# Performance work log

Hardware: AMD Instinct MI355X
Metric: run time of the kernel (lower is better)

Reference implementation:

```python
import jax, jax.numpy as jnp
import numpy as np

NUM_GRAPHS = 64


def gcn_conv(x, src, dst, num_nodes, W, b):
    # PyG GCNConv: linear first, then normalized aggregation, bias after.
    h = x @ W  # [N, out]
    # degree with self-loops already included in (src, dst)
    deg = jax.ops.segment_sum(jnp.ones_like(src, dtype=h.dtype), dst, num_segments=num_nodes)
    dinv = jnp.where(deg > 0, jax.lax.rsqrt(jnp.maximum(deg, 1e-12)), 0.0)
    norm = dinv[src] * dinv[dst]  # [E]
    msg = h[src] * norm[:, None]  # [E, out] gather + scale
    out = jax.ops.segment_sum(msg, dst, num_segments=num_nodes)  # scatter-add
    return out + b


def setup_inputs() -> dict:
    key = jax.random.key(0)
    ks = jax.random.split(key, 12)
    N, E = 50000, 400000
    dims = [36, 75, 150, 50]
    x = jax.random.normal(ks[0], (N, dims[0]), dtype=jnp.float32)
    edge_index = jax.random.randint(ks[1], (2, E), 0, N, dtype=jnp.int64)
    batch = jnp.sort(jax.random.randint(ks[2], (N,), 0, NUM_GRAPHS, dtype=jnp.int64))
    def glorot(k, fi, fo):
        lim = np.sqrt(6.0 / (fi + fo)).astype(np.float32)
        return jax.random.uniform(k, (fi, fo), jnp.float32, -lim, lim)
    inp = {"x": x, "edge_index": edge_index, "batch": batch}
    for i in range(3):
        inp[f"W{i+1}"] = glorot(ks[3 + 2 * i], dims[i], dims[i + 1])
        inp[f"b{i+1}"] = jnp.zeros((dims[i + 1],), jnp.float32)
    inp["Wo"] = glorot(ks[9], dims[3], 3)
    inp["bo"] = jnp.zeros((3,), jnp.float32)
    return inp


def reference(x, edge_index, batch, W1, b1, W2, b2, W3, b3, Wo, bo):
    N = x.shape[0]
    loop = jnp.arange(N, dtype=edge_index.dtype)
    src = jnp.concatenate([edge_index[0], loop])  # add self-loops
    dst = jnp.concatenate([edge_index[1], loop])
    h = x
    for W, b in ((W1, b1), (W2, b2), (W3, b3)):
        h = gcn_conv(h, src, dst, N, W, b)
        h = jax.nn.relu(h)  # dropout is identity in eval mode
    h = h @ Wo + bo  # [N, 3]
    pooled = jax.ops.segment_max(h, batch, num_segments=NUM_GRAPHS)  # [G, 3]
    return jax.nn.softmax(pooled, axis=1)
```

## Files before the change

### kernel.cpp

```cpp
#include <hip/hip_runtime.h>
#include <hip/hip_bf16.h>

#define DIV_UP(a, b) (((a) + (b) - 1) / (b))
typedef long long ll;
typedef __attribute__((ext_vector_type(8))) short short8;
typedef __attribute__((ext_vector_type(4))) float f32x4;

__device__ __forceinline__ float ldf(const void* p, ll i, int bf) {
    return bf ? __bfloat162float(((const __hip_bfloat16*)p)[i]) : ((const float*)p)[i];
}
__device__ __forceinline__ int ldi(const int* p, ll i, int w) {
    return w ? p[2 * i] : p[i];
}
template <int MODE>
__device__ __forceinline__ float ldm(const void* p, ll i, int bf) {
    if (MODE == 1) return __bfloat162float(((const __hip_bfloat16*)p)[i]);
    return ldf(p, i, bf);
}
__device__ __forceinline__ void bf16pair(unsigned u, float& f0, float& f1) {
    f0 = __uint_as_float(u << 16);
    f1 = __uint_as_float(u & 0xFFFF0000u);
}

__device__ __forceinline__ unsigned fenc(float f) {
    unsigned u = __float_as_uint(f);
    return (u & 0x80000000u) ? ~u : (u | 0x80000000u);
}
__device__ __forceinline__ float fdec(unsigned u) {
    unsigned v = (u & 0x80000000u) ? (u & 0x7FFFFFFFu) : ~u;
    return __uint_as_float(v);
}
#define ENC_NEG_INF 0x007FFFFFu

#define MB1 0
#define MB2 80
#define MHW 240
#define MB3 390
#define MBO 440
#define N_MISC 444
#define P1 0
#define P2 5120
#define P3 20480
#define N_PACK 30720

__global__ void k_detect(const unsigned* __restrict__ xb, const unsigned* __restrict__ eb,
                         int* __restrict__ flags, int* __restrict__ cnt, int N) {
    int idx = blockIdx.x * 256 + threadIdx.x;
    if (idx < N) cnt[idx] = 0;
    if (blockIdx.x != 0) return;
    __shared__ int sv[2];
    int t = threadIdx.x;
    if (t < 2) sv[t] = 0;
    __syncthreads();
    unsigned e = (xb[t] >> 7) & 0xFFu;
    int vote = (e >= 115u && e <= 133u) ? 1 : 0;
    int zero = (eb[2 * t + 1] == 0u) ? 1 : 0;
    atomicAdd(&sv[0], vote);
    atomicAdd(&sv[1], zero);
    __syncthreads();
    if (t == 0) {
        flags[0] = (sv[0] > 128) ? 1 : 0;
        flags[1] = (sv[1] > 200) ? 1 : 0;
    }
}

__global__ void k_cvt(const void* __restrict__ W1, const void* __restrict__ b1,
                      const void* __restrict__ W2, const void* __restrict__ b2,
                      const void* __restrict__ W3, const void* __restrict__ b3,
                      const void* __restrict__ Wo, const void* __restrict__ bo,
                      __hip_bfloat16* __restrict__ wp, float* __restrict__ wfm,
                      const int* __restrict__ flags) {
    int t = blockIdx.x * blockDim.x + threadIdx.x;
    int bf = flags[0];
    if (t < N_PACK) {
        const void* W;
        int i, K, OUT, KC;
        if (t < P2) {
            W = W1;
            i = t;
            K = 36;
            OUT = 75;
            KC = 2;
        } else if (t < P3) {
            W = W2;
            i = t - P2;
            K = 75;
            OUT = 150;
            KC = 3;
        } else {
            W = W3;
            i = t - P3;
            K = 150;
            OUT = 50;
            KC = 5;
        }
        int j = i & 7;
        int lane = (i >> 3) & 63;
        int tile = i >> 9;
        int kc = tile % KC;
        int ct = tile / KC;
        int k = kc * 32 + ((lane >> 4) << 3) + j;
        int col = ct * 16 + (lane & 15);
        float v = (k < K && col < OUT) ? ldf(W, (ll)k * OUT + col, bf) : 0.0f;
        wp[t] = __float2bfloat16(v);
    } else {
        int m = t - N_PACK;
        if (m >= N_MISC) return;
        float v = 0.0f;
        if (m < 75)
            v = ldf(b1, m, bf);
        else if (m >= MB2 && m < MB2 + 150)
            v = ldf(b2, m - MB2, bf);
        else if (m >= MHW && m < MHW + 150)
            v = ldf(Wo, m - MHW, bf);
        else if (m >= MB3 && m < MB3 + 50)
            v = ldf(b3, m - MB3, bf);
        else if (m >= MBO && m < MBO + 3)
            v = ldf(bo, m - MBO, bf);
        wfm[m] = v;
    }
}

__global__ void k_hist(const int* __restrict__ ei, int* __restrict__ cnt,
                       const int* __restrict__ flags, int E) {
    int t = blockIdx.x * blockDim.x + threadIdx.x;
    if (t >= E) return;
    atomicAdd(&cnt[ldi(ei, (ll)E + t, flags[1])], 1);
}
__global__ void k_scan1(const int* __restrict__ cnt, int* __restrict__ bsum,
                        float* __restrict__ dinv, int N) {
    __shared__ int s[256];
    int t = threadIdx.x;
    int idx = blockIdx.x * 256 + t;
    int v = (idx < N) ? cnt[idx] : 0;
    if (idx < N) dinv[idx] = rsqrtf((float)v + 1.0f);
    s[t] = v;
    __syncthreads();
#pragma unroll
    for (int off = 128; off > 0; off >>= 1) {
        if (t < off) s[t] += s[t + off];
        __syncthreads();
    }
    if (t == 0) bsum[blockIdx.x] = s[0];
}
__global__ void k_scan2(int* __restrict__ bsum, int nb, unsigned* __restrict__ pooled) {
    __shared__ int s[256];
    int t = threadIdx.x;
    if (t < 192) pooled[t] = ENC_NEG_INF;
    int run = 0;
    for (int base = 0; base < nb; base += 256) {
        int i = base + t;
        int v = (i < nb) ? bsum[i] : 0;
        s[t] = v;
        __syncthreads();
        for (int off = 1; off < 256; off <<= 1) {
            int o = (t >= off) ? s[t - off] : 0;
            __syncthreads();
            s[t] += o;
            __syncthreads();
        }
        if (i < nb) bsum[i] = run + s[t] - v;
        run += s[255];
        __syncthreads();
    }
}
__global__ void k_scan3(int* __restrict__ cnt, const int* __restrict__ bsum,
                        int* __restrict__ rowptr, int N) {
    __shared__ int s[256];
    int t = threadIdx.x;
    int idx = blockIdx.x * 256 + t;
    int v = (idx < N) ? cnt[idx] : 0;
    if (idx < N) cnt[idx] = 0;
    s[t] = v;
    __syncthreads();
    for (int off = 1; off < 256; off <<= 1) {
        int o = (t >= off) ? s[t - off] : 0;
        __syncthreads();
        s[t] += o;
        __syncthreads();
    }
    if (idx <= N) rowptr[idx] = bsum[blockIdx.x] + s[t] - v;
}
__global__ void k_fill(const int* __restrict__ ei, const int* __restrict__ rowptr,
                       int* __restrict__ cursor, int2* __restrict__ ep,
                       const float* __restrict__ dinv, const int* __restrict__ flags, int E) {
    int t = blockIdx.x * blockDim.x + threadIdx.x;
    if (t >= E) return;
    int wi = flags[1];
    int s = ldi(ei, t, wi);
    int d = ldi(ei, (ll)E + t, wi);
    int pos = rowptr[d] + atomicAdd(&cursor[d], 1);
    int2 v;
    v.x = s;
    v.y = __float_as_int(dinv[s] * dinv[d]);
    ep[pos] = v;
}

__global__ void k_agg(const void* __restrict__ X, int xstride, __hip_bfloat16* __restrict__ Y,
                      int ystride, int C, const int* __restrict__ rowptr,
                      const int2* __restrict__ ep, const float* __restrict__ dinv,
                      const int* __restrict__ flags, int N) {
    int n = blockIdx.x * 4 + (threadIdx.x >> 6);
    if (n >= N) return;
    int lane = threadIdx.x & 63;
    int bf = flags[0];
    float di = dinv[n];
    float w0 = di * di;
    if (lane >= C) return;
    float a0 = w0 * ldm<2>(X, (ll)n * xstride + lane, bf);
    int j = rowptr[n];
    int je = rowptr[n + 1];
    for (; j + 3 < je; j += 4) {
        int2 v0 = ep[j];
        int2 v1 = ep[j + 1];
        int2 v2 = ep[j + 2];
        int2 v3 = ep[j + 3];
        a0 = fmaf(__int_as_float(v0.y), ldm<2>(X, (ll)v0.x * xstride + lane, bf), a0);
        a0 = fmaf(__int_as_float(v1.y), ldm<2>(X, (ll)v1.x * xstride + lane, bf), a0);
        a0 = fmaf(__int_as_float(v2.y), ldm<2>(X, (ll)v2.x * xstride + lane, bf), a0);
        a0 = fmaf(__int_as_float(v3.y), ldm<2>(X, (ll)v3.x * xstride + lane, bf), a0);
    }
    for (; j < je; ++j) {
        int2 v0 = ep[j];
        a0 = fmaf(__int_as_float(v0.y), ldm<2>(X, (ll)v0.x * xstride + lane, bf), a0);
    }
    Y[(ll)n * ystride + lane] = __float2bfloat16(a0);
}

__global__ void k_aggp(const __hip_bfloat16* __restrict__ X, int xs,
                       __hip_bfloat16* __restrict__ Y, int ys, int CP,
                       const int* __restrict__ rowptr, const int2* __restrict__ ep,
                       const float* __restrict__ dinv, int N) {
    int n = blockIdx.x * 4 + (threadIdx.x >> 6);
    if (n >= N) return;
    int lane = threadIdx.x & 63;
    if (lane >= CP) return;
    float di = dinv[n];
    float w0 = di * di;
    float a0, a1;
    {
        unsigned u = *(const unsigned*)(X + (ll)n * xs + 2 * lane);
        float f0, f1;
        bf16pair(u, f0, f1);
        a0 = w0 * f0;
        a1 = w0 * f1;
    }
    int j = rowptr[n];
    int je = rowptr[n + 1];
    for (; j + 3 < je; j += 4) {
        int2 v0 = ep[j];
        int2 v1 = ep[j + 1];
        int2 v2 = ep[j + 2];
        int2 v3 = ep[j + 3];
        unsigned u0 = *(const unsigned*)(X + (ll)v0.x * xs + 2 * lane);
        unsigned u1 = *(const unsigned*)(X + (ll)v1.x * xs + 2 * lane);
        unsigned u2 = *(const unsigned*)(X + (ll)v2.x * xs + 2 * lane);
        unsigned u3 = *(const unsigned*)(X + (ll)v3.x * xs + 2 * lane);
        float f0, f1;
        bf16pair(u0, f0, f1);
        float wa = __int_as_float(v0.y);
        a0 = fmaf(wa, f0, a0);
        a1 = fmaf(wa, f1, a1);
        bf16pair(u1, f0, f1);
        wa = __int_as_float(v1.y);
        a0 = fmaf(wa, f0, a0);
        a1 = fmaf(wa, f1, a1);
        bf16pair(u2, f0, f1);
        wa = __int_as_float(v2.y);
        a0 = fmaf(wa, f0, a0);
        a1 = fmaf(wa, f1, a1);
        bf16pair(u3, f0, f1);
        wa = __int_as_float(v3.y);
        a0 = fmaf(wa, f0, a0);
        a1 = fmaf(wa, f1, a1);
    }
    for (; j < je; ++j) {
        int2 v0 = ep[j];
        unsigned u = *(const unsigned*)(X + (ll)v0.x * xs + 2 * lane);
        float f0, f1;
        bf16pair(u, f0, f1);
        float wa = __int_as_float(v0.y);
        a0 = fmaf(wa, f0, a0);
        a1 = fmaf(wa, f1, a1);
    }
    __hip_bfloat162 h;
    h.x = __float2bfloat16(a0);
    h.y = __float2bfloat16(a1);
    *(__hip_bfloat162*)(Y + (ll)n * ys + 2 * lane) = h;
}

__global__ void k_agg3h(const __hip_bfloat16* __restrict__ X, int xs, float* __restrict__ zb,
                        const int* __restrict__ rowptr, const int2* __restrict__ ep,
                        const float* __restrict__ dinv, const float* __restrict__ wfm, int N) {
    int n = blockIdx.x * 4 + (threadIdx.x >> 6);
    if (n >= N) return;
    int lane = threadIdx.x & 63;
    bool act = lane < 25;
    int c0 = 2 * lane;
    float w00 = 0, w01 = 0, w02 = 0, w10 = 0, w11 = 0, w12 = 0, bb0 = 0, bb1 = 0;
    if (act) {
        w00 = wfm[MHW + c0 * 3 + 0];
        w01 = wfm[MHW + c0 * 3 + 1];
        w02 = wfm[MHW + c0 * 3 + 2];
        w10 = wfm[MHW + c0 * 3 + 3];
        w11 = wfm[MHW + c0 * 3 + 4];
        w12 = wfm[MHW + c0 * 3 + 5];
        bb0 = wfm[MB3 + c0];
        bb1 = wfm[MB3 + c0 + 1];
    }
    float di = dinv[n];
    float w0 = di * di;
    float a0 = 0.0f, a1 = 0.0f;
    if (act) {
        unsigned u = *(const unsigned*)(X + (ll)n * xs + 2 * lane);
        float f0, f1;
        bf16pair(u, f0, f1);
        a0 = w0 * f0;
        a1 = w0 * f1;
    }
    int j = rowptr[n];
    int je = rowptr[n + 1];
    for (; j + 3 < je; j += 4) {
        int2 v0 = ep[j];
        int2 v1 = ep[j + 1];
        int2 v2 = ep[j + 2];
        int2 v3 = ep[j + 3];
        if (act) {
            unsigned u0 = *(const unsigned*)(X + (ll)v0.x * xs + 2 * lane);
            unsigned u1 = *(const unsigned*)(X + (ll)v1.x * xs + 2 * lane);
            unsigned u2 = *(const unsigned*)(X + (ll)v2.x * xs + 2 * lane);
            unsigned u3 = *(const unsigned*)(X + (ll)v3.x * xs + 2 * lane);
            float f0, f1;
            bf16pair(u0, f0, f1);
            float wa = __int_as_float(v0.y);
            a0 = fmaf(wa, f0, a0);
            a1 = fmaf(wa, f1, a1);
            bf16pair(u1, f0, f1);
            wa = __int_as_float(v1.y);
            a0 = fmaf(wa, f0, a0);
            a1 = fmaf(wa, f1, a1);
            bf16pair(u2, f0, f1);
            wa = __int_as_float(v2.y);
            a0 = fmaf(wa, f0, a0);
            a1 = fmaf(wa, f1, a1);
            bf16pair(u3, f0, f1);
            wa = __int_as_float(v3.y);
            a0 = fmaf(wa, f0, a0);
            a1 = fmaf(wa, f1, a1);
        }
    }
    for (; j < je; ++j) {
        int2 v0 = ep[j];
        if (act) {
            unsigned u = *(const unsigned*)(X + (ll)v0.x * xs + 2 * lane);
            float f0, f1;
            bf16pair(u, f0, f1);
            float wa = __int_as_float(v0.y);
            a0 = fmaf(wa, f0, a0);
            a1 = fmaf(wa, f1, a1);
        }
    }
    float h0 = act ? fmaxf(a0 + bb0, 0.0f) : 0.0f;
    float h1 = act ? fmaxf(a1 + bb1, 0.0f) : 0.0f;
    float z0 = h0 * w00 + h1 * w10;
    float z1 = h0 * w01 + h1 * w11;
    float z2 = h0 * w02 + h1 * w12;
#pragma unroll
    for (int off = 32; off > 0; off >>= 1) {
        z0 += __shfl_xor(z0, off);
        z1 += __shfl_xor(z1, off);
        z2 += __shfl_xor(z2, off);
    }
    if (lane == 0) {
        zb[(ll)n * 3 + 0] = z0 + wfm[MBO + 0];
        zb[(ll)n * 3 + 1] = z1 + wfm[MBO + 1];
        zb[(ll)n * 3 + 2] = z2 + wfm[MBO + 2];
    }
}

template <int K, int KC, int OUT, int CT, bool RELU, bool BIAS>
__global__ __launch_bounds__(256) void k_gemm(const __hip_bfloat16* __restrict__ X, int xs,
                                              __hip_bfloat16* __restrict__ Y, int ys,
                                              const short8* __restrict__ Wp,
                                              const float* __restrict__ bias, int N) {
    const int lane = threadIdx.x & 63;
    const int wid = threadIdx.x >> 6;
    const int m0 = blockIdx.x * 64 + wid * 16;
    const int mrow = lane & 15;
    const int koct = lane >> 4;
    const __hip_bfloat16* xrow = X + (ll)(m0 + mrow) * xs + koct * 8;
    f32x4 acc[CT];
#pragma unroll
    for (int ct = 0; ct < CT; ++ct)
#pragma unroll
        for (int r = 0; r < 4; ++r) acc[ct][r] = 0.0f;
    float bv[CT];
#pragma unroll
    for (int ct = 0; ct < CT; ++ct) {
        int col = ct * 16 + mrow;
        bv[ct] = (BIAS && col < OUT) ? bias[col] : 0.0f;
    }
#pragma unroll 1
    for (int kc = 0; kc < KC; ++kc) {
        short8 a = *(const short8*)(xrow + kc * 32);
#pragma unroll
        for (int ct = 0; ct < CT; ++ct) {
            short8 b = Wp[(ct * KC + kc) * 64 + lane];
            acc[ct] = __builtin_amdgcn_mfma_f32_16x16x32_bf16(a, b, acc[ct], 0, 0, 0);
        }
    }
#pragma unroll
    for (int ct = 0; ct < CT; ++ct) {
        int col = ct * 16 + mrow;
        if (col >= OUT) continue;
#pragma unroll
        for (int r = 0; r < 4; ++r) {
            int node = m0 + koct * 4 + r;
            if (node >= N) continue;
            float v = acc[ct][r] + bv[ct];
            if (RELU) v = fmaxf(v, 0.0f);
            Y[(ll)node * ys + col] = __float2bfloat16(v);
        }
    }
}

__global__ void k_pool(const float* __restrict__ zb, const int* __restrict__ batch,
                       unsigned* __restrict__ pooled, const int* __restrict__ flags, int N) {
    __shared__ unsigned lmax[192];
    int wi = flags[1];
    for (int i = threadIdx.x; i < 192; i += blockDim.x) lmax[i] = ENC_NEG_INF;
    __syncthreads();
    int n = blockIdx.x * blockDim.x + threadIdx.x;
    int lane = threadIdx.x & 63;
    float z0 = -3.4e38f, z1 = -3.4e38f, z2 = -3.4e38f;
    int g = 0;
    if (n < N) {
        z0 = zb[(ll)n * 3 + 0];
        z1 = zb[(ll)n * 3 + 1];
        z2 = zb[(ll)n * 3 + 2];
        g = ldi(batch, n, wi);
    }
    int g0 = __shfl(g, 0);
    unsigned long long uni = __ballot(n < N && g == g0);
    if (uni == ~0ULL) {
#pragma unroll
        for (int off = 32; off > 0; off >>= 1) {
            z0 = fmaxf(z0, __shfl_xor(z0, off));
            z1 = fmaxf(z1, __shfl_xor(z1, off));
            z2 = fmaxf(z2, __shfl_xor(z2, off));
        }
        if (lane == 0) {
            atomicMax(&lmax[g0 * 3 + 0], fenc(z0));
            atomicMax(&lmax[g0 * 3 + 1], fenc(z1));
            atomicMax(&lmax[g0 * 3 + 2], fenc(z2));
        }
    } else if (n < N) {
        atomicMax(&lmax[g * 3 + 0], fenc(z0));
        atomicMax(&lmax[g * 3 + 1], fenc(z1));
        atomicMax(&lmax[g * 3 + 2], fenc(z2));
    }
    __syncthreads();
    for (int i = threadIdx.x; i < 192; i += blockDim.x) {
        unsigned v = lmax[i];
        if (v != ENC_NEG_INF) atomicMax(&pooled[i], v);
    }
}

__global__ void k_softmax(const unsigned* __restrict__ pooled, void* __restrict__ out,
                          const int* __restrict__ flags) {
    int g = threadIdx.x;
    if (g >= 64) return;
    int bf = flags[0];
    float a = fdec(pooled[g * 3 + 0]);
    float b = fdec(pooled[g * 3 + 1]);
    float c = fdec(pooled[g * 3 + 2]);
    float m = fmaxf(a, fmaxf(b, c));
    float ea = __expf(a - m), eb = __expf(b - m), ec = __expf(c - m);
    float s = 1.0f / (ea + eb + ec);
    if (bf) {
        __hip_bfloat16* o = (__hip_bfloat16*)out;
        o[g * 3 + 0] = __float2bfloat16(ea * s);
        o[g * 3 + 1] = __float2bfloat16(eb * s);
        o[g * 3 + 2] = __float2bfloat16(ec * s);
    } else {
        float* o = (float*)out;
        o[g * 3 + 0] = ea * s;
        o[g * 3 + 1] = eb * s;
        o[g * 3 + 2] = ec * s;
    }
}

extern "C" void kernel_launch(void* const* d_in, const int* in_sizes, int n_in,
                              void* d_out, int out_size, void* d_ws, size_t ws_size,
                              hipStream_t stream) {
    const void* x = d_in[0];
    const int* ei = (const int*)d_in[1];
    const int* batch = (const int*)d_in[2];

    const int N = in_sizes[0] / 36;
    const int E = in_sizes[1] / 2;

    char* ws = (char*)d_ws;
    size_t off = 0;
    auto carve = [&](size_t bytes) {
        char* p = ws + off;
        off = (off + bytes + 255) & ~(size_t)255;
        return p;
    };
    int* flags = (int*)carve(16);
    float* wfm = (float*)carve((size_t)N_MISC * 4);
    __hip_bfloat16* wpack = (__hip_bfloat16*)carve((size_t)N_PACK * 2);
    float* dinv = (float*)carve((size_t)N * 4);
    int* cnt = (int*)carve((size_t)N * 4);
    int* rowptr = (int*)carve((size_t)(N + 1) * 4);
    int2* ep = (int2*)carve((size_t)E * 8);
    unsigned* pooled = (unsigned*)carve(768);
    const int NB = DIV_UP(N + 1, 256);
    int* bsum = (int*)carve((size_t)NB * 4);
    float* zbuf = (float*)carve((size_t)N * 12);
    char* R1 = carve((size_t)N * 192);
    char* R2 = carve((size_t)N * 320);
    (void)carve(65536);

    const int B = 256;
    const int GB = DIV_UP(N, 64);

    k_detect<<<DIV_UP(N, B), B, 0, stream>>>((const unsigned*)x, (const unsigned*)ei, flags, cnt,
                                             N);
    k_cvt<<<DIV_UP(N_PACK + N_MISC, B), B, 0, stream>>>(d_in[3], d_in[4], d_in[5], d_in[6],
                                                        d_in[7], d_in[8], d_in[9], d_in[10], wpack,
                                                        wfm, flags);

    k_hist<<<DIV_UP(E, B), B, 0, stream>>>(ei, cnt, flags, E);
    k_scan1<<<NB, 256, 0, stream>>>(cnt, bsum, dinv, N);
    k_scan2<<<1, 256, 0, stream>>>(bsum, NB, pooled);
    k_scan3<<<NB, 256, 0, stream>>>(cnt, bsum, rowptr, N);
    k_fill<<<DIV_UP(E, B), B, 0, stream>>>(ei, rowptr, cnt, ep, dinv, flags, E);

    k_agg<<<DIV_UP(N, 4), B, 0, stream>>>(x, 36, (__hip_bfloat16*)R1, 64, 36, rowptr, ep, dinv,
                                          flags, N);
    k_gemm<36, 2, 75, 5, true, true><<<GB, B, 0, stream>>>(
        (const __hip_bfloat16*)R1, 64, (__hip_bfloat16*)R2, 80, (const short8*)(wpack + P1),
        wfm + MB1, N);

    k_aggp<<<DIV_UP(N, 4), B, 0, stream>>>((const __hip_bfloat16*)R2, 80, (__hip_bfloat16*)R1, 96,
                                           38, rowptr, ep, dinv, N);
    k_gemm<75, 3, 150, 10, true, true><<<GB, B, 0, stream>>>(
        (const __hip_bfloat16*)R1, 96, (__hip_bfloat16*)R2, 160, (const short8*)(wpack + P2),
        wfm + MB2, N);

    k_gemm<150, 5, 50, 4, false, false><<<GB, B, 0, stream>>>(
        (const __hip_bfloat16*)R2, 160, (__hip_bfloat16*)R1, 64, (const short8*)(wpack + P3), wfm,
        N);
    k_agg3h<<<DIV_UP(N, 4), B, 0, stream>>>((const __hip_bfloat16*)R1, 64, zbuf, rowptr, ep, dinv,
                                            wfm, N);

    k_pool<<<DIV_UP(N, B), B, 0, stream>>>(zbuf, batch, pooled, flags, N);
    k_softmax<<<1, 64, 0, stream>>>(pooled, d_out, flags);
}
```

Baseline: 254.8 us.

## Aggregate one node per half-wavefront in all three GCN aggregation kernels

Each of the three sparse aggregation kernels now maps one node to 32 lanes instead of 64, so a 256-thread block covers eight nodes rather than four. Lanes that previously sat idle, since the widest row uses at most 38 lanes, now process another node. The layer-1 kernel gains a packed bf16-pair path and splits the fp32 path into two column halves. The layer-2 kernel handles 76 columns with one main bf16 pair per lane plus a second pair on six lanes. The cost is more divergence between the two half-waves when node degrees differ, plus extra predicated loads.

Result: faster. 238.5 us (-6.4%).

```diff
diff --git a/kernel.cpp b/kernel.cpp
--- a/kernel.cpp
+++ b/kernel.cpp
@@ -11,11 +11,6 @@
 }
 __device__ __forceinline__ int ldi(const int* p, ll i, int w) {
     return w ? p[2 * i] : p[i];
-}
-template <int MODE>
-__device__ __forceinline__ float ldm(const void* p, ll i, int bf) {
-    if (MODE == 1) return __bfloat162float(((const __hip_bfloat16*)p)[i]);
-    return ldf(p, i, bf);
 }
 __device__ __forceinline__ void bf16pair(unsigned u, float& f0, float& f1) {
     f0 = __uint_as_float(u << 16);
@@ -196,105 +191,175 @@
     ep[pos] = v;
 }
 
-__global__ void k_agg(const void* __restrict__ X, int xstride, __hip_bfloat16* __restrict__ Y,
-                      int ystride, int C, const int* __restrict__ rowptr,
-                      const int2* __restrict__ ep, const float* __restrict__ dinv,
-                      const int* __restrict__ flags, int N) {
-    int n = blockIdx.x * 4 + (threadIdx.x >> 6);
+__global__ void k_agg1(const void* __restrict__ X, __hip_bfloat16* __restrict__ Y,
+                       const int* __restrict__ rowptr, const int2* __restrict__ ep,
+                       const float* __restrict__ dinv, const int* __restrict__ flags, int N) {
+    int n = blockIdx.x * 8 + (threadIdx.x >> 5);
     if (n >= N) return;
-    int lane = threadIdx.x & 63;
+    int lane = threadIdx.x & 31;
     int bf = flags[0];
     float di = dinv[n];
     float w0 = di * di;
-    if (lane >= C) return;
-    float a0 = w0 * ldm<2>(X, (ll)n * xstride + lane, bf);
     int j = rowptr[n];
     int je = rowptr[n + 1];
-    for (; j + 3 < je; j += 4) {
+    if (bf) {
+        const __hip_bfloat16* Xb = (const __hip_bfloat16*)X;
+        bool act = lane < 18;
+        float a0 = 0.0f, a1 = 0.0f;
+        if (act) {
+            float f0, f1;
+            bf16pair(*(const unsigned*)(Xb + (ll)n * 36 + 2 * lane), f0, f1);
+            a0 = w0 * f0;
+            a1 = w0 * f1;
+        }
+        for (; j + 3 < je; j += 4) {
+            int2 v0 = ep[j];
+            int2 v1 = ep[j + 1];
+            int2 v2 = ep[j + 2];
+            int2 v3 = ep[j + 3];
+            if (act) {
+                float f0, f1;
+                bf16pair(*(const unsigned*)(Xb + (ll)v0.x * 36 + 2 * lane), f0, f1);
+                float wa = __int_as_float(v0.y);
+                a0 = fmaf(wa, f0, a0);
+                a1 = fmaf(wa, f1, a1);
+                bf16pair(*(const unsigned*)(Xb + (ll)v1.x * 36 + 2 * lane), f0, f1);
+                wa = __int_as_float(v1.y);
+                a0 = fmaf(wa, f0, a0);
+                a1 = fmaf(wa, f1, a1);
+                bf16pair(*(const unsigned*)(Xb + (ll)v2.x * 36 + 2 * lane), f0, f1);
+                wa = __int_as_float(v2.y);
+                a0 = fmaf(wa, f0, a0);
+                a1 = fmaf(wa, f1, a1);
+                bf16pair(*(const unsigned*)(Xb + (ll)v3.x * 36 + 2 * lane), f0, f1);
+                wa = __int_as_float(v3.y);
+                a0 = fmaf(wa, f0, a0);
+                a1 = fmaf(wa, f1, a1);
+            }
+        }
+        for (; j < je; ++j) {
+            int2 v0 = ep[j];
+            if (act) {
+                float f0, f1;
+                bf16pair(*(const unsigned*)(Xb + (ll)v0.x * 36 + 2 * lane), f0, f1);
+                float wa = __int_as_float(v0.y);
+                a0 = fmaf(wa, f0, a0);
+                a1 = fmaf(wa, f1, a1);
+            }
+        }
+        if (act) {
+            __hip_bfloat162 h;
+            h.x = __float2bfloat16(a0);
+            h.y = __float2bfloat16(a1);
+            *(__hip_bfloat162*)(Y + (ll)n * 64 + 2 * lane) = h;
+        }
+    } else {
+        const float* Xf = (const float*)X;
+        bool act2 = lane < 4;
+        float a0 = w0 * Xf[(ll)n * 36 + lane];
+        float a1 = act2 ? w0 * Xf[(ll)n * 36 + 32 + lane] : 0.0f;
+        for (; j + 3 < je; j += 4) {
+            int2 v0 = ep[j];
+            int2 v1 = ep[j + 1];
+            int2 v2 = ep[j + 2];
+            int2 v3 = ep[j + 3];
+            float wa = __int_as_float(v0.y);
+            a0 = fmaf(wa, Xf[(ll)v0.x * 36 + lane], a0);
+            if (act2) a1 = fmaf(wa, Xf[(ll)v0.x * 36 + 32 + lane], a1);
+            wa = __int_as_float(v1.y);
+            a0 = fmaf(wa, Xf[(ll)v1.x * 36 + lane], a0);
+            if (act2) a1 = fmaf(wa, Xf[(ll)v1.x * 36 + 32 + lane], a1);
+            wa = __int_as_float(v2.y);
+            a0 = fmaf(wa, Xf[(ll)v2.x * 36 + lane], a0);
+            if (act2) a1 = fmaf(wa, Xf[(ll)v2.x * 36 + 32 + lane], a1);
+            wa = __int_as_float(v3.y);
+            a0 = fmaf(wa, Xf[(ll)v3.x * 36 + lane], a0);
+            if (act2) a1 = fmaf(wa, Xf[(ll)v3.x * 36 + 32 + lane], a1);
+        }
+        for (; j < je; ++j) {
+            int2 v0 = ep[j];
+            float wa = __int_as_float(v0.y);
+            a0 = fmaf(wa, Xf[(ll)v0.x * 36 + lane], a0);
+            if (act2) a1 = fmaf(wa, Xf[(ll)v0.x * 36 + 32 + lane], a1);
+        }
+        Y[(ll)n * 64 + lane] = __float2bfloat16(a0);
+        if (act2) Y[(ll)n * 64 + 32 + lane] = __float2bfloat16(a1);
+    }
+}
+
+__global__ void k_aggp2(const __hip_bfloat16* __restrict__ X, int xs,
+                        __hip_bfloat16* __restrict__ Y, int ys, const int* __restrict__ rowptr,
+                        const int2* __restrict__ ep, const float* __restrict__ dinv, int N) {
+    int n = blockIdx.x * 8 + (threadIdx.x >> 5);
+    if (n >= N) return;
+    int lane = threadIdx.x & 31;
+    bool act2 = lane < 6;
+    float di = dinv[n];
+    float w0 = di * di;
+    float a0, a1, b0 = 0.0f, b1 = 0.0f;
+    {
+        float f0, f1;
+        bf16pair(*(const unsigned*)(X + (ll)n * xs + 2 * lane), f0, f1);
+        a0 = w0 * f0;
+        a1 = w0 * f1;
+        if (act2) {
+            bf16pair(*(const unsigned*)(X + (ll)n * xs + 64 + 2 * lane), f0, f1);
+            b0 = w0 * f0;
+            b1 = w0 * f1;
+        }
+    }
+    int j = rowptr[n];
+    int je = rowptr[n + 1];
+    for (; j + 1 < je; j += 2) {
         int2 v0 = ep[j];
         int2 v1 = ep[j + 1];
-        int2 v2 = ep[j + 2];
-        int2 v3 = ep[j + 3];
-        a0 = fmaf(__int_as_float(v0.y), ldm<2>(X, (ll)v0.x * xstride + lane, bf), a0);
-        a0 = fmaf(__int_as_float(v1.y), ldm<2>(X, (ll)v1.x * xstride + lane, bf), a0);
-        a0 = fmaf(__int_as_float(v2.y), ldm<2>(X, (ll)v2.x * xstride + lane, bf), a0);
-        a0 = fmaf(__int_as_float(v3.y), ldm<2>(X, (ll)v3.x * xstride + lane, bf), a0);
-    }
-    for (; j < je; ++j) {
-        int2 v0 = ep[j];
-        a0 = fmaf(__int_as_float(v0.y), ldm<2>(X, (ll)v0.x * xstride + lane, bf), a0);
-    }
-    Y[(ll)n * ystride + lane] = __float2bfloat16(a0);
-}
-
-__global__ void k_aggp(const __hip_bfloat16* __restrict__ X, int xs,
-                       __hip_bfloat16* __restrict__ Y, int ys, int CP,
-                       const int* __restrict__ rowptr, const int2* __restrict__ ep,
-                       const float* __restrict__ dinv, int N) {
-    int n = blockIdx.x * 4 + (threadIdx.x >> 6);
-    if (n >= N) return;
-    int lane = threadIdx.x & 63;
-    if (lane >= CP) return;
-    float di = dinv[n];
-    float w0 = di * di;
-    float a0, a1;
-    {
-        unsigned u = *(const unsigned*)(X + (ll)n * xs + 2 * lane);
+        float wa = __int_as_float(v0.y), wb = __int_as_float(v1.y);
         float f0, f1;
-        bf16pair(u, f0, f1);
-        a0 = w0 * f0;
-        a1 = w0 * f1;
-    }
-    int j = rowptr[n];
-    int je = rowptr[n + 1];
-    for (; j + 3 < je; j += 4) {
-        int2 v0 = ep[j];
-        int2 v1 = ep[j + 1];
-        int2 v2 = ep[j + 2];
-        int2 v3 = ep[j + 3];
-        unsigned u0 = *(const unsigned*)(X + (ll)v0.x * xs + 2 * lane);
-        unsigned u1 = *(const unsigned*)(X + (ll)v1.x * xs + 2 * lane);
-        unsigned u2 = *(const unsigned*)(X + (ll)v2.x * xs + 2 * lane);
-        unsigned u3 = *(const unsigned*)(X + (ll)v3.x * xs + 2 * lane);
-        float f0, f1;
-        bf16pair(u0, f0, f1);
-        float wa = __int_as_float(v0.y);
+        bf16pair(*(const unsigned*)(X + (ll)v0.x * xs + 2 * lane), f0, f1);
         a0 = fmaf(wa, f0, a0);
         a1 = fmaf(wa, f1, a1);
-        bf16pair(u1, f0, f1);
-        wa = __int_as_float(v1.y);
+        bf16pair(*(const unsigned*)(X + (ll)v1.x * xs + 2 * lane), f0, f1);
+        a0 = fmaf(wb, f0, a0);
+        a1 = fmaf(wb, f1, a1);
+        if (act2) {
+            bf16pair(*(const unsigned*)(X + (ll)v0.x * xs + 64 + 2 * lane), f0, f1);
+            b0 = fmaf(wa, f0, b0);
+            b1 = fmaf(wa, f1, b1);
+            bf16pair(*(const unsigned*)(X + (ll)v1.x * xs + 64 + 2 * lane), f0, f1);
+            b0 = fmaf(wb, f0, b0);
+            b1 = fmaf(wb, f1, b1);
+        }
+    }
+    if (j < je) {
+        int2 v0 = ep[j];
+        float wa = __int_as_float(v0.y);
+        float f0, f1;
+        bf16pair(*(const unsigned*)(X + (ll)v0.x * xs + 2 * lane), f0, f1);
         a0 = fmaf(wa, f0, a0);
         a1 = fmaf(wa, f1, a1);
-        bf16pair(u2, f0, f1);
-        wa = __int_as_float(v2.y);
-        a0 = fmaf(wa, f0, a0);
-        a1 = fmaf(wa, f1, a1);
-        bf16pair(u3, f0, f1);
-        wa = __int_as_float(v3.y);
-        a0 = fmaf(wa, f0, a0);
-        a1 = fmaf(wa, f1, a1);
-    }
-    for (; j < je; ++j) {
-        int2 v0 = ep[j];
-        unsigned u = *(const unsigned*)(X + (ll)v0.x * xs + 2 * lane);
-        float f0, f1;
-        bf16pair(u, f0, f1);
-        float wa = __int_as_float(v0.y);
-        a0 = fmaf(wa, f0, a0);
-        a1 = fmaf(wa, f1, a1);
+        if (act2) {
+            bf16pair(*(const unsigned*)(X + (ll)v0.x * xs + 64 + 2 * lane), f0, f1);
+            b0 = fmaf(wa, f0, b0);
+            b1 = fmaf(wa, f1, b1);
+        }
     }
     __hip_bfloat162 h;
     h.x = __float2bfloat16(a0);
     h.y = __float2bfloat16(a1);
     *(__hip_bfloat162*)(Y + (ll)n * ys + 2 * lane) = h;
+    if (act2) {
+        h.x = __float2bfloat16(b0);
+        h.y = __float2bfloat16(b1);
+        *(__hip_bfloat162*)(Y + (ll)n * ys + 64 + 2 * lane) = h;
+    }
 }
 
 __global__ void k_agg3h(const __hip_bfloat16* __restrict__ X, int xs, float* __restrict__ zb,
                         const int* __restrict__ rowptr, const int2* __restrict__ ep,
                         const float* __restrict__ dinv, const float* __restrict__ wfm, int N) {
-    int n = blockIdx.x * 4 + (threadIdx.x >> 6);
+    int n = blockIdx.x * 8 + (threadIdx.x >> 5);
     if (n >= N) return;
-    int lane = threadIdx.x & 63;
+    int lane = threadIdx.x & 31;
     bool act = lane < 25;
     int c0 = 2 * lane;
     float w00 = 0, w01 = 0, w02 = 0, w10 = 0, w11 = 0, w12 = 0, bb0 = 0, bb1 = 0;
@@ -312,9 +377,8 @@
     float w0 = di * di;
     float a0 = 0.0f, a1 = 0.0f;
     if (act) {
-        unsigned u = *(const unsigned*)(X + (ll)n * xs + 2 * lane);
         float f0, f1;
-        bf16pair(u, f0, f1);
+        bf16pair(*(const unsigned*)(X + (ll)n * xs + 2 * lane), f0, f1);
         a0 = w0 * f0;
         a1 = w0 * f1;
     }
@@ -326,24 +390,20 @@
         int2 v2 = ep[j + 2];
         int2 v3 = ep[j + 3];
         if (act) {
-            unsigned u0 = *(const unsigned*)(X + (ll)v0.x * xs + 2 * lane);
-            unsigned u1 = *(const unsigned*)(X + (ll)v1.x * xs + 2 * lane);
-            unsigned u2 = *(const unsigned*)(X + (ll)v2.x * xs + 2 * lane);
-            unsigned u3 = *(const unsigned*)(X + (ll)v3.x * xs + 2 * lane);
             float f0, f1;
-            bf16pair(u0, f0, f1);
+            bf16pair(*(const unsigned*)(X + (ll)v0.x * xs + 2 * lane), f0, f1);
             float wa = __int_as_float(v0.y);
             a0 = fmaf(wa, f0, a0);
             a1 = fmaf(wa, f1, a1);
-            bf16pair(u1, f0, f1);
+            bf16pair(*(const unsigned*)(X + (ll)v1.x * xs + 2 * lane), f0, f1);
             wa = __int_as_float(v1.y);
             a0 = fmaf(wa, f0, a0);
             a1 = fmaf(wa, f1, a1);
-            bf16pair(u2, f0, f1);
+            bf16pair(*(const unsigned*)(X + (ll)v2.x * xs + 2 * lane), f0, f1);
             wa = __int_as_float(v2.y);
             a0 = fmaf(wa, f0, a0);
             a1 = fmaf(wa, f1, a1);
-            bf16pair(u3, f0, f1);
+            bf16pair(*(const unsigned*)(X + (ll)v3.x * xs + 2 * lane), f0, f1);
             wa = __int_as_float(v3.y);
             a0 = fmaf(wa, f0, a0);
             a1 = fmaf(wa, f1, a1);
@@ -352,9 +412,8 @@
     for (; j < je; ++j) {
         int2 v0 = ep[j];
         if (act) {
-            unsigned u = *(const unsigned*)(X + (ll)v0.x * xs + 2 * lane);
             float f0, f1;
-            bf16pair(u, f0, f1);
+            bf16pair(*(const unsigned*)(X + (ll)v0.x * xs + 2 * lane), f0, f1);
             float wa = __int_as_float(v0.y);
             a0 = fmaf(wa, f0, a0);
             a1 = fmaf(wa, f1, a1);
@@ -366,7 +425,7 @@
     float z1 = h0 * w01 + h1 * w11;
     float z2 = h0 * w02 + h1 * w12;
 #pragma unroll
-    for (int off = 32; off > 0; off >>= 1) {
+    for (int off = 16; off > 0; off >>= 1) {
         z0 += __shfl_xor(z0, off);
         z1 += __shfl_xor(z1, off);
         z2 += __shfl_xor(z2, off);
@@ -537,14 +596,13 @@
     k_scan3<<<NB, 256, 0, stream>>>(cnt, bsum, rowptr, N);
     k_fill<<<DIV_UP(E, B), B, 0, stream>>>(ei, rowptr, cnt, ep, dinv, flags, E);
 
-    k_agg<<<DIV_UP(N, 4), B, 0, stream>>>(x, 36, (__hip_bfloat16*)R1, 64, 36, rowptr, ep, dinv,
-                                          flags, N);
+    k_agg1<<<DIV_UP(N, 8), B, 0, stream>>>(x, (__hip_bfloat16*)R1, rowptr, ep, dinv, flags, N);
     k_gemm<36, 2, 75, 5, true, true><<<GB, B, 0, stream>>>(
         (const __hip_bfloat16*)R1, 64, (__hip_bfloat16*)R2, 80, (const short8*)(wpack + P1),
         wfm + MB1, N);
 
-    k_aggp<<<DIV_UP(N, 4), B, 0, stream>>>((const __hip_bfloat16*)R2, 80, (__hip_bfloat16*)R1, 96,
-                                           38, rowptr, ep, dinv, N);
+    k_aggp2<<<DIV_UP(N, 8), B, 0, stream>>>((const __hip_bfloat16*)R2, 80, (__hip_bfloat16*)R1, 96,
+                                            rowptr, ep, dinv, N);
     k_gemm<75, 3, 150, 10, true, true><<<GB, B, 0, stream>>>(
         (const __hip_bfloat16*)R1, 96, (__hip_bfloat16*)R2, 160, (const short8*)(wpack + P2),
         wfm + MB2, N);
@@ -552,7 +610,7 @@
     k_gemm<150, 5, 50, 4, false, false><<<GB, B, 0, stream>>>(
         (const __hip_bfloat16*)R2, 160, (__hip_bfloat16*)R1, 64, (const short8*)(wpack + P3), wfm,
         N);
-    k_agg3h<<<DIV_UP(N, 4), B, 0, stream>>>((const __hip_bfloat16*)R1, 64, zbuf, rowptr, ep, dinv,
+    k_agg3h<<<DIV_UP(N, 8), B, 0, stream>>>((const __hip_bfloat16*)R1, 64, zbuf, rowptr, ep, dinv,
                                             wfm, N);
 
     k_pool<<<DIV_UP(N, B), B, 0, stream>>>(zbuf, batch, pooled, flags, N);
```
